# Optimization experiments

Hardware: AMD Instinct MI355X
Metric: run time of the kernel (lower is better)

The kernel has to match this reference:

```python
import jax, jax.numpy as jnp
import numpy as np

WAY = 5
SHOT = 5
SCALE = 10.0
EPS = 1e-8


def setup_inputs() -> dict:
    key = jax.random.key(0)
    k1, k2 = jax.random.split(key, 2)
    x = jax.random.normal(k1, (100, 512, 16, 16), dtype=jnp.float32)
    W = jax.random.normal(k2, (512, 512), dtype=jnp.float32) * 0.02  # 1x1 conv weight (outC, inC)
    b = jnp.zeros((512,), dtype=jnp.float32)
    return {"x": x, "W": W, "b": b}


def reference(x, W, b):
    B, C, H, Wd = x.shape
    # extract(): 1x1 conv -> softmax over flattened (C*H*W) per sample -> remask
    mask = jnp.einsum('bchw,oc->bohw', x, W) + b[None, :, None, None]
    mask = jax.nn.softmax(mask.reshape(B, -1), axis=1).reshape(B, C, H, Wd)
    x = x * mask
    # predict(): (way, shot+query, C, H, W)
    xv = x.reshape(WAY, -1, C, H, Wd)
    s = xv[:, :SHOT].mean(axis=(1, 3, 4))                    # (m=way, d=C) support prototypes
    q = xv[:, SHOT:].reshape(-1, C, H * Wd)                  # (n, d=C, f=H*W) queries
    # cosine_similarity over d, without materializing (n,m,d,f)
    qn = jnp.maximum(jnp.sqrt(jnp.sum(q * q, axis=1)), EPS)  # (n, f)
    sn = jnp.maximum(jnp.sqrt(jnp.sum(s * s, axis=1)), EPS)  # (m,)
    scores = jnp.einsum('ndf,md->nmf', q, s) / (qn[:, None, :] * sn[None, :, None])
    # softmax over classes (m), then mean over spatial positions f
    return jax.nn.softmax(SCALE * scores, axis=1).mean(axis=2)  # (n, way)
```

## Files before the change

kernel.cpp:

```cpp
#include <hip/hip_runtime.h>
#include <hip/hip_bf16.h>
#include <math.h>

typedef _Float16 half8 __attribute__((ext_vector_type(8)));
typedef float f32x4 __attribute__((ext_vector_type(4)));

#define BATCH 100
#define CH    512
#define HWP   256
#define SAMP  (CH * HWP)

__device__ __forceinline__ void async16(const void* g, void* l) {
  __builtin_amdgcn_global_load_lds(
      (const __attribute__((address_space(1))) unsigned int*)g,
      (__attribute__((address_space(3))) unsigned int*)l, 16, 0, 0);
}

__global__ __launch_bounds__(256) void k_txpose(const float* __restrict__ x,
                                               _Float16* __restrict__ xh,
                                               const float* __restrict__ W,
                                               _Float16* __restrict__ Wh) {
  __shared__ float tb[64][69];
  int bid  = blockIdx.x;
  if (bid >= 3200) {
    int base = (bid - 3200) * 1024 + threadIdx.x;
#pragma unroll
    for (int j = 0; j < 4; j++) Wh[base + j * 256] = (_Float16)W[base + j * 256];
    return;
  }
  int b    = bid >> 5;
  int tile = bid & 31;
  int c0 = (tile >> 2) << 6;
  int p0 = (tile & 3) << 6;
  int t = threadIdx.x;
  const float* xb = x + (size_t)b * SAMP;
#pragma unroll
  for (int it = 0; it < 4; it++) {
    int ch = it * 256 + t;
    int c  = ch >> 4;
    int pc = (ch & 15) << 2;
    float4 v = *(const float4*)(xb + (size_t)(c0 + c) * HWP + p0 + pc);
    tb[c][pc] = v.x; tb[c][pc + 1] = v.y; tb[c][pc + 2] = v.z; tb[c][pc + 3] = v.w;
  }
  __syncthreads();
  _Float16* xhb = xh + (size_t)b * SAMP;
#pragma unroll
  for (int it = 0; it < 2; it++) {
    int ch = it * 256 + t;
    int p  = ch >> 3;
    int ck = (ch & 7) << 3;
    half8 h;
#pragma unroll
    for (int j = 0; j < 8; j++) h[j] = (_Float16)tb[ck + j][p];
    *(half8*)(xhb + (size_t)(p0 + p) * CH + c0 + ck) = h;
  }
}

__global__ __launch_bounds__(256) void k_gemm(const _Float16* __restrict__ Wh,
                                             const _Float16* __restrict__ xh,
                                             const float* __restrict__ bias,
                                             _Float16* __restrict__ u,
                                             float* __restrict__ denom) {
  __shared__ __align__(16) _Float16 smem[128 * 136];
  int bid = blockIdx.x;
  int w     = (bid & 7) * 100 + (bid >> 3);
  int batch = w >> 3;
  int sub   = w & 7;
  int ot = sub & 3, pt = sub >> 2;
  int o0 = ot * 128, p0 = pt * 128;
  const _Float16* Bg = xh + (size_t)batch * SAMP;

  int t  = threadIdx.x;
  int wv = t >> 6, ln = t & 63;
  int qd = ln >> 4, r = ln & 15;
  int wm0 = (wv >> 1) * 64, wn0 = (wv & 1) * 64;

  auto stage = [&](int q, int kk) {
    _Float16* As = smem + q * 8192;
    _Float16* Bs = As + 4096;
#pragma unroll
    for (int it = 0; it < 2; it++) {
      int ch  = it * 256 + t;
      int row = ch >> 2;
      int qc  = ch & 3;
      char* la = (char*)As + (size_t)(it * 256 + wv * 64) * 16;
      char* lb = (char*)Bs + (size_t)(it * 256 + wv * 64) * 16;
      async16((const char*)(Wh + (size_t)(o0 + row) * 512 + kk + qc * 8), la);
      async16((const char*)(Bg + (size_t)(p0 + row) * 512 + kk + qc * 8), lb);
    }
  };

  f32x4 acc[4][4] = {};
  stage(0, 0);
  __syncthreads();

  for (int ks = 0; ks < 16; ks++) {
    int q = ks & 1;
    if (ks < 15) stage(q ^ 1, (ks + 1) * 32);
    const _Float16* As = smem + q * 8192;
    const _Float16* Bs = As + 4096;
    half8 af[4], bf[4];
#pragma unroll
    for (int i = 0; i < 4; i++)
      af[i] = *(const half8*)(As + (wm0 + i * 16 + r) * 32 + qd * 8);
#pragma unroll
    for (int j = 0; j < 4; j++)
      bf[j] = *(const half8*)(Bs + (wn0 + j * 16 + r) * 32 + qd * 8);
#pragma unroll
    for (int i = 0; i < 4; i++)
#pragma unroll
      for (int j = 0; j < 4; j++)
        acc[i][j] = __builtin_amdgcn_mfma_f32_16x16x32_f16(af[i], bf[j], acc[i][j], 0, 0, 0);
    __syncthreads();
  }

#pragma unroll
  for (int it = 0; it < 8; it++) {
    int ch = it * 256 + t;
    int p  = ch >> 4;
    int ck = ch & 15;
    half8 v = *(const half8*)(Bg + (size_t)(p0 + p) * CH + o0 + ck * 8);
    *(half8*)(smem + p * 136 + ck * 8) = v;
  }
  __syncthreads();

  _Float16* outb = u + (size_t)batch * SAMP;
  float lsum = 0.f;
#pragma unroll
  for (int i = 0; i < 4; i++) {
#pragma unroll
    for (int rg = 0; rg < 4; rg++) {
      int ol = wm0 + i * 16 + qd * 4 + rg;
      float bv = bias[o0 + ol];
#pragma unroll
      for (int j = 0; j < 4; j++) {
        int pl = wn0 + j * 16 + r;
        float ev = __expf(acc[i][j][rg] + bv);
        lsum += ev;
        float xv = (float)smem[pl * 136 + ol];
        outb[(size_t)(o0 + ol) * HWP + p0 + pl] = (_Float16)(xv * ev);
      }
    }
  }
#pragma unroll
  for (int off = 32; off; off >>= 1) lsum += __shfl_down(lsum, off, 64);
  __shared__ float rs[4];
  if (ln == 0) rs[wv] = lsum;
  __syncthreads();
  if (t == 0) atomicAdd(&denom[batch], rs[0] + rs[1] + rs[2] + rs[3]);
}

__global__ __launch_bounds__(256) void k_proto(const _Float16* __restrict__ u,
                                              const float* __restrict__ denom,
                                              float* __restrict__ sproto) {
  int m = blockIdx.x / 512, c = blockIdx.x % 512;
  int t = threadIdx.x;
  float acc = 0.f;
  for (int j = 0; j < 5; j++) {
    int b = m * 20 + j;
    float invd = 1.0f / denom[b];
    acc += (float)u[(size_t)b * SAMP + (size_t)c * HWP + t] * invd;
  }
#pragma unroll
  for (int off = 32; off; off >>= 1) acc += __shfl_down(acc, off, 64);
  __shared__ float rs[4];
  if ((t & 63) == 0) rs[t >> 6] = acc;
  __syncthreads();
  if (t == 0) sproto[m * 512 + c] = (rs[0] + rs[1] + rs[2] + rs[3]) * (1.0f / 1280.0f);
}

__global__ __launch_bounds__(256) void k_sn(const float* __restrict__ sproto,
                                           float* __restrict__ pref) {
  int m = blockIdx.x, t = threadIdx.x;
  float v1 = sproto[m * 512 + t], v2 = sproto[m * 512 + 256 + t];
  float acc = v1 * v1 + v2 * v2;
#pragma unroll
  for (int off = 32; off; off >>= 1) acc += __shfl_down(acc, off, 64);
  __shared__ float rs[4];
  if ((t & 63) == 0) rs[t >> 6] = acc;
  __syncthreads();
  if (t == 0) {
    float sn = fmaxf(sqrtf(rs[0] + rs[1] + rs[2] + rs[3]), 1e-8f);
    pref[m] = 10.0f / sn;
  }
}

__global__ __launch_bounds__(256) void k_part(const _Float16* __restrict__ u,
                                             const float* __restrict__ sproto,
                                             float* __restrict__ part) {
  __shared__ float s_l[5 * 64];
  int n = blockIdx.x >> 3, gc = blockIdx.x & 7;
  int b = (n / 15) * 20 + 5 + (n % 15);
  int t = threadIdx.x;
  for (int i = t; i < 320; i += 256)
    s_l[i] = sproto[(i >> 6) * 512 + gc * 64 + (i & 63)];
  __syncthreads();
  const _Float16* ub = u + (size_t)b * SAMP + (size_t)gc * 64 * HWP;
  float dot[5] = {0, 0, 0, 0, 0}, qq = 0.f;
#pragma unroll 8
  for (int c = 0; c < 64; c++) {
    float v = (float)ub[c * HWP + t];
    qq += v * v;
#pragma unroll
    for (int m = 0; m < 5; m++) dot[m] += v * s_l[m * 64 + c];
  }
  float* pp = part + (((size_t)n * 8 + gc) * 256 + t) * 6;
  pp[0] = dot[0]; pp[1] = dot[1]; pp[2] = dot[2];
  pp[3] = dot[3]; pp[4] = dot[4]; pp[5] = qq;
}

__global__ __launch_bounds__(256) void k_comb(const float* __restrict__ part,
                                             const float* __restrict__ pref,
                                             float* __restrict__ out) {
  int n = blockIdx.x, t = threadIdx.x;
  float dot[5] = {0, 0, 0, 0, 0}, qq = 0.f;
#pragma unroll
  for (int gc = 0; gc < 8; gc++) {
    const float* pp = part + (((size_t)n * 8 + gc) * 256 + t) * 6;
    dot[0] += pp[0]; dot[1] += pp[1]; dot[2] += pp[2];
    dot[3] += pp[3]; dot[4] += pp[4]; qq += pp[5];
  }
  float iqn = 1.0f / fmaxf(sqrtf(qq), 1e-20f);
  float sc[5], mx = -1e30f;
#pragma unroll
  for (int m = 0; m < 5; m++) { sc[m] = dot[m] * pref[m] * iqn; mx = fmaxf(mx, sc[m]); }
  float p[5], ssum = 0.f;
#pragma unroll
  for (int m = 0; m < 5; m++) { p[m] = __expf(sc[m] - mx); ssum += p[m]; }
  float rr = 1.0f / ssum;
#pragma unroll
  for (int m = 0; m < 5; m++) {
    float v = p[m] * rr;
#pragma unroll
    for (int off = 32; off; off >>= 1) v += __shfl_down(v, off, 64);
    p[m] = v;
  }
  __shared__ float rs[4][5];
  if ((t & 63) == 0) {
#pragma unroll
    for (int m = 0; m < 5; m++) rs[t >> 6][m] = p[m];
  }
  __syncthreads();
  if (t < 5) out[n * 5 + t] =
      (rs[0][t] + rs[1][t] + rs[2][t] + rs[3][t]) * (1.0f / 256.0f);
}

extern "C" void kernel_launch(void* const* d_in, const int* in_sizes, int n_in,
                              void* d_out, int out_size, void* d_ws, size_t ws_size,
                              hipStream_t stream) {
  const float* x    = (const float*)d_in[0];
  const float* W    = (const float*)d_in[1];
  const float* bias = (const float*)d_in[2];
  float* out = (float*)d_out;

  char* ws = (char*)d_ws;
  _Float16* xh     = (_Float16*)(ws + 0);
  float*    part   = (float*)   (ws + 0);
  _Float16* Wh     = (_Float16*)(ws + 26214400);
  _Float16* u      = (_Float16*)(ws + 26738688);
  float*    denom  = (float*)   (ws + 52953088);
  float*    sproto = (float*)   (ws + 52953600);
  float*    pref   = (float*)   (ws + 52963840);

  hipMemsetAsync(denom, 0, 512, stream);
  k_txpose <<<3456, 256, 0, stream>>>(x, xh, W, Wh);
  k_gemm   <<<800,  256, 0, stream>>>(Wh, xh, bias, u, denom);
  k_proto  <<<2560, 256, 0, stream>>>(u, denom, sproto);
  k_sn     <<<5,    256, 0, stream>>>(sproto, pref);
  k_part   <<<600,  256, 0, stream>>>(u, sproto, part);
  k_comb   <<<75,   256, 0, stream>>>(part, pref, out);
}
```

Baseline: 140.0 us.

## Swizzle GEMM LDS tiles, unroll double buffer, merge proto blocks, coalesce partials

The GEMM's LDS tiles now use an XOR swizzle on the 16-byte chunk index, applied on both the async global-to-LDS stores and the fragment reads, to cut bank conflicts. The double-buffer loop is manually unrolled by two with fixed buffer pointers. k_proto now handles all five classes per channel in one block, which reduces launches from 2560 to 512 blocks and shares the denominator loads. The partial-sum layout between k_part and k_comb is changed from interleaved stride-6 to structure-of-arrays so stores and loads coalesce.

```diff
diff --git a/kernel.cpp b/kernel.cpp
--- a/kernel.cpp
+++ b/kernel.cpp
@@ -74,45 +74,58 @@
   int wv = t >> 6, ln = t & 63;
   int qd = ln >> 4, r = ln & 15;
   int wm0 = (wv >> 1) * 64, wn0 = (wv & 1) * 64;
-
-  auto stage = [&](int q, int kk) {
-    _Float16* As = smem + q * 8192;
-    _Float16* Bs = As + 4096;
-#pragma unroll
-    for (int it = 0; it < 2; it++) {
-      int ch  = it * 256 + t;
-      int row = ch >> 2;
-      int qc  = ch & 3;
-      char* la = (char*)As + (size_t)(it * 256 + wv * 64) * 16;
-      char* lb = (char*)Bs + (size_t)(it * 256 + wv * 64) * 16;
-      async16((const char*)(Wh + (size_t)(o0 + row) * 512 + kk + qc * 8), la);
-      async16((const char*)(Bg + (size_t)(p0 + row) * 512 + kk + qc * 8), lb);
-    }
-  };
+  int slr = (qd ^ ((r >> 1) & 3)) << 3;
+
+  _Float16* const A0 = smem;
+  _Float16* const B0 = smem + 4096;
+  _Float16* const A1 = smem + 8192;
+  _Float16* const B1 = smem + 12288;
+
+#define STAGE(As, Bs, kk)                                                     \
+  {                                                                           \
+    _Pragma("unroll")                                                         \
+    for (int it = 0; it < 2; it++) {                                          \
+      int ch  = it * 256 + t;                          \
+      int row = ch >> 2;                                          \
+      int qsw = (ch & 3) ^ ((row >> 1) & 3);    \
+      char* la = (char*)(As) + (size_t)(it * 256 + wv * 64) * 16;             \
+      char* lb = (char*)(Bs) + (size_t)(it * 256 + wv * 64) * 16;             \
+      async16((const char*)(Wh + (size_t)(o0 + row) * 512 + (kk) + qsw * 8), la); \
+      async16((const char*)(Bg + (size_t)(p0 + row) * 512 + (kk) + qsw * 8), lb); \
+    }                                                                         \
+  }
+
+#define COMPUTE(As, Bs)                                                       \
+  {                                                                           \
+    half8 af[4], bf[4];                                                       \
+    _Pragma("unroll")                                                         \
+    for (int i = 0; i < 4; i++)                                               \
+      af[i] = *(const half8*)((As) + (wm0 + i * 16 + r) * 32 + slr);          \
+    _Pragma("unroll")                                                         \
+    for (int j = 0; j < 4; j++)                                               \
+      bf[j] = *(const half8*)((Bs) + (wn0 + j * 16 + r) * 32 + slr);          \
+    _Pragma("unroll")                                                         \
+    for (int i = 0; i < 4; i++)                                               \
+      _Pragma("unroll")                                                       \
+      for (int j = 0; j < 4; j++)                                             \
+        acc[i][j] = __builtin_amdgcn_mfma_f32_16x16x32_f16(af[i], bf[j], acc[i][j], 0, 0, 0); \
+  }
 
   f32x4 acc[4][4] = {};
-  stage(0, 0);
-  __syncthreads();
-
-  for (int ks = 0; ks < 16; ks++) {
-    int q = ks & 1;
-    if (ks < 15) stage(q ^ 1, (ks + 1) * 32);
-    const _Float16* As = smem + q * 8192;
-    const _Float16* Bs = As + 4096;
-    half8 af[4], bf[4];
-#pragma unroll
-    for (int i = 0; i < 4; i++)
-      af[i] = *(const half8*)(As + (wm0 + i * 16 + r) * 32 + qd * 8);
-#pragma unroll
-    for (int j = 0; j < 4; j++)
-      bf[j] = *(const half8*)(Bs + (wn0 + j * 16 + r) * 32 + qd * 8);
-#pragma unroll
-    for (int i = 0; i < 4; i++)
-#pragma unroll
-      for (int j = 0; j < 4; j++)
-        acc[i][j] = __builtin_amdgcn_mfma_f32_16x16x32_f16(af[i], bf[j], acc[i][j], 0, 0, 0);
+  STAGE(A0, B0, 0);
+  __syncthreads();
+
+#pragma unroll 1
+  for (int ks = 0; ks < 16; ks += 2) {
+    STAGE(A1, B1, (ks + 1) * 32);
+    COMPUTE(A0, B0);
     __syncthreads();
-  }
+    if (ks < 14) STAGE(A0, B0, (ks + 2) * 32);
+    COMPUTE(A1, B1);
+    __syncthreads();
+  }
+#undef STAGE
+#undef COMPUTE
 
 #pragma unroll
   for (int it = 0; it < 8; it++) {
@@ -153,20 +166,35 @@
 __global__ __launch_bounds__(256) void k_proto(const _Float16* __restrict__ u,
                                               const float* __restrict__ denom,
                                               float* __restrict__ sproto) {
-  int m = blockIdx.x / 512, c = blockIdx.x % 512;
+  int c = blockIdx.x;
   int t = threadIdx.x;
-  float acc = 0.f;
-  for (int j = 0; j < 5; j++) {
-    int b = m * 20 + j;
-    float invd = 1.0f / denom[b];
-    acc += (float)u[(size_t)b * SAMP + (size_t)c * HWP + t] * invd;
-  }
-#pragma unroll
-  for (int off = 32; off; off >>= 1) acc += __shfl_down(acc, off, 64);
-  __shared__ float rs[4];
-  if ((t & 63) == 0) rs[t >> 6] = acc;
-  __syncthreads();
-  if (t == 0) sproto[m * 512 + c] = (rs[0] + rs[1] + rs[2] + rs[3]) * (1.0f / 1280.0f);
+  int wv = t >> 6;
+  float accm[5];
+#pragma unroll
+  for (int m = 0; m < 5; m++) {
+    float acc = 0.f;
+#pragma unroll
+    for (int j = 0; j < 5; j++) {
+      int b = m * 20 + j;
+      acc += (float)u[(size_t)b * SAMP + (size_t)c * HWP + t] * (1.0f / denom[b]);
+    }
+    accm[m] = acc;
+  }
+#pragma unroll
+  for (int m = 0; m < 5; m++) {
+    float v = accm[m];
+#pragma unroll
+    for (int off = 32; off; off >>= 1) v += __shfl_down(v, off, 64);
+    accm[m] = v;
+  }
+  __shared__ float rs[4][5];
+  if ((t & 63) == 0) {
+#pragma unroll
+    for (int m = 0; m < 5; m++) rs[wv][m] = accm[m];
+  }
+  __syncthreads();
+  if (t < 5) sproto[t * 512 + c] =
+      (rs[0][t] + rs[1][t] + rs[2][t] + rs[3][t]) * (1.0f / 1280.0f);
 }
 
 __global__ __launch_bounds__(256) void k_sn(const float* __restrict__ sproto,
@@ -204,9 +232,9 @@
 #pragma unroll
     for (int m = 0; m < 5; m++) dot[m] += v * s_l[m * 64 + c];
   }
-  float* pp = part + (((size_t)n * 8 + gc) * 256 + t) * 6;
-  pp[0] = dot[0]; pp[1] = dot[1]; pp[2] = dot[2];
-  pp[3] = dot[3]; pp[4] = dot[4]; pp[5] = qq;
+  float* pp = part + (size_t)(n * 8 + gc) * 6 * 256 + t;
+  pp[0 * 256] = dot[0]; pp[1 * 256] = dot[1]; pp[2 * 256] = dot[2];
+  pp[3 * 256] = dot[3]; pp[4 * 256] = dot[4]; pp[5 * 256] = qq;
 }
 
 __global__ __launch_bounds__(256) void k_comb(const float* __restrict__ part,
@@ -216,9 +244,9 @@
   float dot[5] = {0, 0, 0, 0, 0}, qq = 0.f;
 #pragma unroll
   for (int gc = 0; gc < 8; gc++) {
-    const float* pp = part + (((size_t)n * 8 + gc) * 256 + t) * 6;
-    dot[0] += pp[0]; dot[1] += pp[1]; dot[2] += pp[2];
-    dot[3] += pp[3]; dot[4] += pp[4]; qq += pp[5];
+    const float* pp = part + (size_t)(n * 8 + gc) * 6 * 256 + t;
+    dot[0] += pp[0 * 256]; dot[1] += pp[1 * 256]; dot[2] += pp[2 * 256];
+    dot[3] += pp[3 * 256]; dot[4] += pp[4 * 256]; qq += pp[5 * 256];
   }
   float iqn = 1.0f / fmaxf(sqrtf(qq), 1e-20f);
   float sc[5], mx = -1e30f;
@@ -265,7 +293,7 @@
   hipMemsetAsync(denom, 0, 512, stream);
   k_txpose <<<3456, 256, 0, stream>>>(x, xh, W, Wh);
   k_gemm   <<<800,  256, 0, stream>>>(Wh, xh, bias, u, denom);
-  k_proto  <<<2560, 256, 0, stream>>>(u, denom, sproto);
+  k_proto  <<<512,  256, 0, stream>>>(u, denom, sproto);
   k_sn     <<<5,    256, 0, stream>>>(sproto, pref);
   k_part   <<<600,  256, 0, stream>>>(u, sproto, part);
   k_comb   <<<75,   256, 0, stream>>>(part, pref, out);
```

Result: no change. 137.4 us (-1.9%).

## Fold memset and k_sn into neighbors, swizzle GEMM epilogue LDS, regroup proto/part kernels

Applied to the files above, without the earlier changes.

Removes the memset by zeroing denom inside the transpose kernel, and removes k_sn by computing the prototype norms inside k_comb. This trims launch overhead. The GEMM epilogue switches from padded LDS to an XOR-swizzled layout, which shrinks shared memory to allow an occupancy hint of 5. It also does per-wave atomics instead of a block reduction. k_proto now handles all 5 classes per block, and k_part processes 4 positions per thread with half4 loads and a coalesced SoA partial layout, which cuts block counts. Each comb block redundantly recomputes the norms, and k_part now has fewer blocks (150), so parallelism drops.

```diff
diff --git a/kernel.cpp b/kernel.cpp
--- a/kernel.cpp
+++ b/kernel.cpp
@@ -3,6 +3,7 @@
 #include <math.h>
 
 typedef _Float16 half8 __attribute__((ext_vector_type(8)));
+typedef _Float16 half4 __attribute__((ext_vector_type(4)));
 typedef float f32x4 __attribute__((ext_vector_type(4)));
 
 #define BATCH 100
@@ -19,13 +20,15 @@
 __global__ __launch_bounds__(256) void k_txpose(const float* __restrict__ x,
                                                _Float16* __restrict__ xh,
                                                const float* __restrict__ W,
-                                               _Float16* __restrict__ Wh) {
+                                               _Float16* __restrict__ Wh,
+                                               float* __restrict__ denom) {
   __shared__ float tb[64][69];
   int bid  = blockIdx.x;
   if (bid >= 3200) {
     int base = (bid - 3200) * 1024 + threadIdx.x;
 #pragma unroll
     for (int j = 0; j < 4; j++) Wh[base + j * 256] = (_Float16)W[base + j * 256];
+    if (bid == 3200 && threadIdx.x < 128) denom[threadIdx.x] = 0.0f;
     return;
   }
   int b    = bid >> 5;
@@ -56,12 +59,12 @@
   }
 }
 
-__global__ __launch_bounds__(256) void k_gemm(const _Float16* __restrict__ Wh,
-                                             const _Float16* __restrict__ xh,
-                                             const float* __restrict__ bias,
-                                             _Float16* __restrict__ u,
-                                             float* __restrict__ denom) {
-  __shared__ __align__(16) _Float16 smem[128 * 136];
+__global__ __launch_bounds__(256, 5) void k_gemm(const _Float16* __restrict__ Wh,
+                                                 const _Float16* __restrict__ xh,
+                                                 const float* __restrict__ bias,
+                                                 _Float16* __restrict__ u,
+                                                 float* __restrict__ denom) {
+  __shared__ __align__(16) _Float16 smem[16384];
   int bid = blockIdx.x;
   int w     = (bid & 7) * 100 + (bid >> 3);
   int batch = w >> 3;
@@ -120,7 +123,7 @@
     int p  = ch >> 4;
     int ck = ch & 15;
     half8 v = *(const half8*)(Bg + (size_t)(p0 + p) * CH + o0 + ck * 8);
-    *(half8*)(smem + p * 136 + ck * 8) = v;
+    *(half8*)(smem + p * 128 + ((ck ^ (p & 7)) << 3)) = v;
   }
   __syncthreads();
 
@@ -132,98 +135,136 @@
     for (int rg = 0; rg < 4; rg++) {
       int ol = wm0 + i * 16 + qd * 4 + rg;
       float bv = bias[o0 + ol];
+      int lo = ol >> 3, wo = ol & 7;
 #pragma unroll
       for (int j = 0; j < 4; j++) {
         int pl = wn0 + j * 16 + r;
         float ev = __expf(acc[i][j][rg] + bv);
         lsum += ev;
-        float xv = (float)smem[pl * 136 + ol];
+        float xv = (float)smem[pl * 128 + ((lo ^ (pl & 7)) << 3) + wo];
         outb[(size_t)(o0 + ol) * HWP + p0 + pl] = (_Float16)(xv * ev);
       }
     }
   }
 #pragma unroll
   for (int off = 32; off; off >>= 1) lsum += __shfl_down(lsum, off, 64);
-  __shared__ float rs[4];
-  if (ln == 0) rs[wv] = lsum;
-  __syncthreads();
-  if (t == 0) atomicAdd(&denom[batch], rs[0] + rs[1] + rs[2] + rs[3]);
+  if (ln == 0) atomicAdd(&denom[batch], lsum);
 }
 
 __global__ __launch_bounds__(256) void k_proto(const _Float16* __restrict__ u,
                                               const float* __restrict__ denom,
                                               float* __restrict__ sproto) {
-  int m = blockIdx.x / 512, c = blockIdx.x % 512;
+  int c = blockIdx.x;
   int t = threadIdx.x;
-  float acc = 0.f;
-  for (int j = 0; j < 5; j++) {
-    int b = m * 20 + j;
-    float invd = 1.0f / denom[b];
-    acc += (float)u[(size_t)b * SAMP + (size_t)c * HWP + t] * invd;
-  }
-#pragma unroll
-  for (int off = 32; off; off >>= 1) acc += __shfl_down(acc, off, 64);
-  __shared__ float rs[4];
-  if ((t & 63) == 0) rs[t >> 6] = acc;
-  __syncthreads();
-  if (t == 0) sproto[m * 512 + c] = (rs[0] + rs[1] + rs[2] + rs[3]) * (1.0f / 1280.0f);
-}
-
-__global__ __launch_bounds__(256) void k_sn(const float* __restrict__ sproto,
-                                           float* __restrict__ pref) {
-  int m = blockIdx.x, t = threadIdx.x;
-  float v1 = sproto[m * 512 + t], v2 = sproto[m * 512 + 256 + t];
-  float acc = v1 * v1 + v2 * v2;
-#pragma unroll
-  for (int off = 32; off; off >>= 1) acc += __shfl_down(acc, off, 64);
-  __shared__ float rs[4];
-  if ((t & 63) == 0) rs[t >> 6] = acc;
-  __syncthreads();
-  if (t == 0) {
-    float sn = fmaxf(sqrtf(rs[0] + rs[1] + rs[2] + rs[3]), 1e-8f);
-    pref[m] = 10.0f / sn;
-  }
+  int wv = t >> 6;
+  float accm[5];
+#pragma unroll
+  for (int m = 0; m < 5; m++) {
+    float acc = 0.f;
+#pragma unroll
+    for (int j = 0; j < 5; j++) {
+      int b = m * 20 + j;
+      acc += (float)u[(size_t)b * SAMP + (size_t)c * HWP + t] * (1.0f / denom[b]);
+    }
+    accm[m] = acc;
+  }
+#pragma unroll
+  for (int m = 0; m < 5; m++) {
+    float v = accm[m];
+#pragma unroll
+    for (int off = 32; off; off >>= 1) v += __shfl_down(v, off, 64);
+    accm[m] = v;
+  }
+  __shared__ float rs[4][5];
+  if ((t & 63) == 0) {
+#pragma unroll
+    for (int m = 0; m < 5; m++) rs[wv][m] = accm[m];
+  }
+  __syncthreads();
+  if (t < 5) sproto[t * 512 + c] =
+      (rs[0][t] + rs[1][t] + rs[2][t] + rs[3][t]) * (1.0f / 1280.0f);
 }
 
 __global__ __launch_bounds__(256) void k_part(const _Float16* __restrict__ u,
                                              const float* __restrict__ sproto,
                                              float* __restrict__ part) {
-  __shared__ float s_l[5 * 64];
-  int n = blockIdx.x >> 3, gc = blockIdx.x & 7;
+  __shared__ float s_l[5 * 256];
+  int n = blockIdx.x >> 1, gq = blockIdx.x & 1;
   int b = (n / 15) * 20 + 5 + (n % 15);
   int t = threadIdx.x;
-  for (int i = t; i < 320; i += 256)
-    s_l[i] = sproto[(i >> 6) * 512 + gc * 64 + (i & 63)];
-  __syncthreads();
-  const _Float16* ub = u + (size_t)b * SAMP + (size_t)gc * 64 * HWP;
-  float dot[5] = {0, 0, 0, 0, 0}, qq = 0.f;
-#pragma unroll 8
+  int gcl = t >> 6;
+  int gc  = gq * 4 + gcl;
+  int pq  = (t & 63) << 2;
+  for (int i = t; i < 1280; i += 256)
+    s_l[i] = sproto[(i >> 8) * 512 + gq * 256 + (i & 255)];
+  __syncthreads();
+  const _Float16* ub = u + (size_t)b * SAMP + (size_t)gc * 64 * HWP + pq;
+  float dot[5][4] = {}, qq[4] = {0, 0, 0, 0};
+#pragma unroll 4
   for (int c = 0; c < 64; c++) {
-    float v = (float)ub[c * HWP + t];
-    qq += v * v;
-#pragma unroll
-    for (int m = 0; m < 5; m++) dot[m] += v * s_l[m * 64 + c];
-  }
-  float* pp = part + (((size_t)n * 8 + gc) * 256 + t) * 6;
-  pp[0] = dot[0]; pp[1] = dot[1]; pp[2] = dot[2];
-  pp[3] = dot[3]; pp[4] = dot[4]; pp[5] = qq;
+    half4 v = *(const half4*)(ub + c * HWP);
+    float sv[5];
+#pragma unroll
+    for (int m = 0; m < 5; m++) sv[m] = s_l[m * 256 + gcl * 64 + c];
+#pragma unroll
+    for (int k = 0; k < 4; k++) {
+      float val = (float)v[k];
+      qq[k] += val * val;
+#pragma unroll
+      for (int m = 0; m < 5; m++) dot[m][k] += val * sv[m];
+    }
+  }
+  float* pp = part + (size_t)(n * 8 + gc) * 6 * 256 + pq;
+#pragma unroll
+  for (int m = 0; m < 5; m++) {
+    float4 o; o.x = dot[m][0]; o.y = dot[m][1]; o.z = dot[m][2]; o.w = dot[m][3];
+    *(float4*)(pp + m * 256) = o;
+  }
+  float4 oq; oq.x = qq[0]; oq.y = qq[1]; oq.z = qq[2]; oq.w = qq[3];
+  *(float4*)(pp + 5 * 256) = oq;
 }
 
 __global__ __launch_bounds__(256) void k_comb(const float* __restrict__ part,
-                                             const float* __restrict__ pref,
+                                             const float* __restrict__ sproto,
                                              float* __restrict__ out) {
   int n = blockIdx.x, t = threadIdx.x;
+  int wv = t >> 6;
+  __shared__ float prefs[5];
+  __shared__ float rsn[4][5];
+  {
+    float sn2[5];
+#pragma unroll
+    for (int m = 0; m < 5; m++) {
+      float v1 = sproto[m * 512 + t], v2 = sproto[m * 512 + 256 + t];
+      sn2[m] = v1 * v1 + v2 * v2;
+    }
+#pragma unroll
+    for (int m = 0; m < 5; m++) {
+      float v = sn2[m];
+#pragma unroll
+      for (int off = 32; off; off >>= 1) v += __shfl_down(v, off, 64);
+      sn2[m] = v;
+    }
+    if ((t & 63) == 0) {
+#pragma unroll
+      for (int m = 0; m < 5; m++) rsn[wv][m] = sn2[m];
+    }
+    __syncthreads();
+    if (t < 5) prefs[t] =
+        10.0f / fmaxf(sqrtf(rsn[0][t] + rsn[1][t] + rsn[2][t] + rsn[3][t]), 1e-8f);
+    __syncthreads();
+  }
   float dot[5] = {0, 0, 0, 0, 0}, qq = 0.f;
 #pragma unroll
   for (int gc = 0; gc < 8; gc++) {
-    const float* pp = part + (((size_t)n * 8 + gc) * 256 + t) * 6;
-    dot[0] += pp[0]; dot[1] += pp[1]; dot[2] += pp[2];
-    dot[3] += pp[3]; dot[4] += pp[4]; qq += pp[5];
+    const float* pp = part + (size_t)(n * 8 + gc) * 6 * 256 + t;
+    dot[0] += pp[0 * 256]; dot[1] += pp[1 * 256]; dot[2] += pp[2 * 256];
+    dot[3] += pp[3 * 256]; dot[4] += pp[4 * 256]; qq += pp[5 * 256];
   }
   float iqn = 1.0f / fmaxf(sqrtf(qq), 1e-20f);
   float sc[5], mx = -1e30f;
 #pragma unroll
-  for (int m = 0; m < 5; m++) { sc[m] = dot[m] * pref[m] * iqn; mx = fmaxf(mx, sc[m]); }
+  for (int m = 0; m < 5; m++) { sc[m] = dot[m] * prefs[m] * iqn; mx = fmaxf(mx, sc[m]); }
   float p[5], ssum = 0.f;
 #pragma unroll
   for (int m = 0; m < 5; m++) { p[m] = __expf(sc[m] - mx); ssum += p[m]; }
@@ -260,13 +301,10 @@
   _Float16* u      = (_Float16*)(ws + 26738688);
   float*    denom  = (float*)   (ws + 52953088);
   float*    sproto = (float*)   (ws + 52953600);
-  float*    pref   = (float*)   (ws + 52963840);
-
-  hipMemsetAsync(denom, 0, 512, stream);
-  k_txpose <<<3456, 256, 0, stream>>>(x, xh, W, Wh);
+
+  k_txpose <<<3456, 256, 0, stream>>>(x, xh, W, Wh, denom);
   k_gemm   <<<800,  256, 0, stream>>>(Wh, xh, bias, u, denom);
-  k_proto  <<<2560, 256, 0, stream>>>(u, denom, sproto);
-  k_sn     <<<5,    256, 0, stream>>>(sproto, pref);
-  k_part   <<<600,  256, 0, stream>>>(u, sproto, part);
-  k_comb   <<<75,   256, 0, stream>>>(part, pref, out);
-}
+  k_proto  <<<512,  256, 0, stream>>>(u, denom, sproto);
+  k_part   <<<150,  256, 0, stream>>>(u, sproto, part);
+  k_comb   <<<75,   256, 0, stream>>>(part, sproto, out);
+}
```

Measured after the change: 169.1 us. 1.21x slower.
